# Optimization experiments

Hardware: AMD Instinct MI355X
Metric: run time of the kernel (lower is better)

Reference implementation:

```python
import jax, jax.numpy as jnp
import numpy as np

B, N, D_MODEL = 8, 1024, 512
H, DK = 8, 64
STATIONS = 128
MASK_NEG = -1e9
LN_EPS = 1e-6


def setup_inputs() -> dict:
    key = jax.random.key(0)
    ks = jax.random.split(key, 9)
    return {
        "hidden_states": jax.random.normal(ks[0], (B, N, D_MODEL), dtype=jnp.float32),
        "rpe": jax.random.normal(ks[1], (B, H, N, N), dtype=jnp.float32) * 0.1,
        "Wq": jax.random.normal(ks[2], (H * DK, D_MODEL), dtype=jnp.float32) * 0.02,
        "Wk": jax.random.normal(ks[3], (H * DK, D_MODEL), dtype=jnp.float32) * 0.02,
        "Wv": jax.random.normal(ks[4], (H * DK, D_MODEL), dtype=jnp.float32) * 0.02,
        "fc_w": jax.random.normal(ks[5], (D_MODEL, H * DK), dtype=jnp.float32) * 0.02,
        "fc_b": jnp.zeros((D_MODEL,), dtype=jnp.float32),
        "ln_g": jnp.ones((D_MODEL,), dtype=jnp.float32),
        "ln_b": jnp.zeros((D_MODEL,), dtype=jnp.float32),
    }


def _star_mask(n, stations):
    # q_k_mask: query i attends to key j iff j < stations or i == j
    idx = jnp.arange(n)
    return (idx[None, :] < stations) | (idx[:, None] == idx[None, :])  # [n, n] bool


def reference(hidden_states, rpe, Wq, Wk, Wv, fc_w, fc_b, ln_g, ln_b):
    b, n, _ = hidden_states.shape
    residual = hidden_states
    q = (hidden_states @ Wq.T).reshape(b, n, H, DK)
    k = (hidden_states @ Wk.T).reshape(b, n, H, DK)
    v = (hidden_states @ Wv.T).reshape(b, n, H, DK)
    # sparse star+self-loop QK^T with inline RPE add (dense emulation of QKP_mm_tvm)
    scores = jnp.einsum("bihd,bjhd->bhij", q, k) + rpe  # [b,h,n,n]
    mask = _star_mask(n, STATIONS)
    scores = jnp.where(mask[None, None], scores, MASK_NEG)
    scores = scores / jnp.sqrt(jnp.float32(DK))
    attn = jax.nn.softmax(scores, axis=-1)
    # AttnV_mm_tvm: sparse attn-weights times V
    ctx = jnp.einsum("bhij,bjhd->bihd", attn, v).reshape(b, n, H * DK)
    ctx = ctx @ fc_w.T + fc_b + residual
    mu = jnp.mean(ctx, axis=-1, keepdims=True)
    var = jnp.var(ctx, axis=-1, keepdims=True)
    return (ctx - mu) / jnp.sqrt(var + LN_EPS) * ln_g + ln_b
```

## Files before the change

### kernel.cpp

```cpp
#include <hip/hip_runtime.h>
#include <hip/hip_bf16.h>
#include <math.h>

#define B_  8
#define N_  1024
#define DM  512
#define H_  8
#define DK_ 64
#define ST  128

typedef __attribute__((ext_vector_type(8))) short short8;
typedef __attribute__((ext_vector_type(4))) float floatx4;

#define GLD16(gp, lp)                                                          \
    __builtin_amdgcn_global_load_lds(                                          \
        (const __attribute__((address_space(1))) void*)(gp),                   \
        (__attribute__((address_space(3))) void*)(lp), 16, 0, 0)

__device__ __forceinline__ float b2f(short u) {
    union { unsigned int i; float f; } c;
    c.i = ((unsigned int)(unsigned short)u) << 16;
    return c.f;
}
__device__ __forceinline__ unsigned short f2b(float f) {
    __hip_bfloat16 t = __float2bfloat16(f);
    return *(unsigned short*)&t;
}

struct CastArgs {
    const float* src[5];
    unsigned short* dst[5];
    int n[5];
};

__global__ __launch_bounds__(256)
void cast_bf16_kernel(CastArgs a)
{
    const int j = blockIdx.y;
    const float* __restrict__ s = a.src[j];
    unsigned short* __restrict__ d = a.dst[j];
    const int n = a.n[j];
    int i = (blockIdx.x * 256 + threadIdx.x) * 8;
    if (i >= n) return;
    float4 x0 = *(const float4*)&s[i];
    float4 x1 = *(const float4*)&s[i + 4];
    ushort4 o0, o1;
    o0.x = f2b(x0.x); o0.y = f2b(x0.y); o0.z = f2b(x0.z); o0.w = f2b(x0.w);
    o1.x = f2b(x1.x); o1.y = f2b(x1.y); o1.z = f2b(x1.z); o1.w = f2b(x1.w);
    *(ushort4*)&d[i] = o0;
    *(ushort4*)&d[i + 4] = o1;
}

__device__ __forceinline__
void gemm_core(const unsigned short* __restrict__ A,
               const unsigned short* __restrict__ W,
               int m0, int n0, unsigned short* As, unsigned short* Bs,
               floatx4 acc[4][4])
{
    const int tid = threadIdx.x;
    const int lane = tid & 63;
    const int wave = tid >> 6;
    const int wm = wave >> 1, wn = wave & 1;
    const int srow = tid >> 2;
    const int skq  = (tid & 3) * 8;
    const unsigned short* Ag = A + (size_t)(m0 + srow) * 512 + skq;
    const unsigned short* Bg = W + (size_t)(n0 + srow) * 512 + skq;
    const int mrow = lane & 15;
    const int koff = (lane >> 4) * 8;

    for (int kt = 0; kt < 512; kt += 32) {
        __syncthreads();
        GLD16(Ag + kt,            &As[tid * 8]);
        GLD16(Ag + 64 * 512 + kt, &As[2048 + tid * 8]);
        GLD16(Bg + kt,            &Bs[tid * 8]);
        GLD16(Bg + 64 * 512 + kt, &Bs[2048 + tid * 8]);
        __syncthreads();
        short8 af[4], bf[4];
        #pragma unroll
        for (int t = 0; t < 4; ++t) {
            af[t] = *(const short8*)&As[(wm * 64 + t * 16 + mrow) * 32 + koff];
            bf[t] = *(const short8*)&Bs[(wn * 64 + t * 16 + mrow) * 32 + koff];
        }
        #pragma unroll
        for (int mt = 0; mt < 4; ++mt)
            #pragma unroll
            for (int nt = 0; nt < 4; ++nt)
                acc[mt][nt] = __builtin_amdgcn_mfma_f32_16x16x32_bf16(
                    af[mt], bf[nt], acc[mt][nt], 0, 0, 0);
    }
}

__global__ __launch_bounds__(256)
void qkv_gemm_kernel(const unsigned short* __restrict__ A,
                     const unsigned short* __restrict__ W0,
                     const unsigned short* __restrict__ W1,
                     const unsigned short* __restrict__ W2,
                     unsigned short* __restrict__ qo,
                     unsigned short* __restrict__ ko,
                     unsigned short* __restrict__ vto)
{
    __shared__ __align__(16) unsigned short As[128 * 32];
    __shared__ __align__(16) unsigned short Bs[128 * 32];
    const int by = blockIdx.y;
    const int sel = by >> 2;
    const unsigned short* W = (sel == 0) ? W0 : (sel == 1 ? W1 : W2);
    const int m0 = blockIdx.x * 128;
    const int n0 = (by & 3) * 128;

    floatx4 acc[4][4];
    #pragma unroll
    for (int i = 0; i < 4; ++i)
        #pragma unroll
        for (int j = 0; j < 4; ++j)
            acc[i][j] = (floatx4){0.f, 0.f, 0.f, 0.f};

    gemm_core(A, W, m0, n0, As, Bs, acc);

    const int lane = threadIdx.x & 63;
    const int wave = threadIdx.x >> 6;
    const int wm = wave >> 1, wn = wave & 1;
    const int lx = lane & 15;
    const int rq = (lane >> 4) * 4;

    if (sel == 2) {
        #pragma unroll
        for (int mt = 0; mt < 4; ++mt) {
            const int mrow = m0 + wm * 64 + mt * 16 + rq;
            const int bb = mrow >> 10, tok = mrow & 1023;
            #pragma unroll
            for (int nt = 0; nt < 4; ++nt) {
                const int c = n0 + wn * 64 + nt * 16 + lx;
                const int hh = c >> 6, d = c & 63;
                ushort4 pk;
                pk.x = f2b(acc[mt][nt][0]); pk.y = f2b(acc[mt][nt][1]);
                pk.z = f2b(acc[mt][nt][2]); pk.w = f2b(acc[mt][nt][3]);
                *(ushort4*)&vto[((size_t)(bb * H_ + hh) * DK_ + d) * N_ + tok] = pk;
            }
        }
    } else {
        unsigned short* O = (sel == 0) ? qo : ko;
        #pragma unroll
        for (int mt = 0; mt < 4; ++mt) {
            const int mrow = m0 + wm * 64 + mt * 16 + rq;
            const int bb = mrow >> 10, tok = mrow & 1023;
            #pragma unroll
            for (int nt = 0; nt < 4; ++nt) {
                const int c = n0 + wn * 64 + nt * 16 + lx;
                const int hh = c >> 6, d = c & 63;
                unsigned short* p =
                    O + ((size_t)(bb * H_ + hh) * N_ + tok) * DK_ + d;
                #pragma unroll
                for (int r = 0; r < 4; ++r)
                    p[(size_t)r * DK_] = f2b(acc[mt][nt][r]);
            }
        }
    }
}

__global__ __launch_bounds__(256)
void fc_gemm_kernel(const unsigned short* __restrict__ A,
                    const unsigned short* __restrict__ W,
                    const float* __restrict__ bias,
                    const float* __restrict__ resid,
                    float* __restrict__ C)
{
    __shared__ __align__(16) unsigned short As[128 * 32];
    __shared__ __align__(16) unsigned short Bs[128 * 32];
    const int m0 = blockIdx.x * 128;
    const int n0 = blockIdx.y * 128;

    floatx4 acc[4][4];
    #pragma unroll
    for (int i = 0; i < 4; ++i)
        #pragma unroll
        for (int j = 0; j < 4; ++j)
            acc[i][j] = (floatx4){0.f, 0.f, 0.f, 0.f};

    gemm_core(A, W, m0, n0, As, Bs, acc);

    const int lane = threadIdx.x & 63;
    const int wave = threadIdx.x >> 6;
    const int wm = wave >> 1, wn = wave & 1;
    const int col = n0 + wn * 64 + (lane & 15);
    const int rq  = (lane >> 4) * 4;
    #pragma unroll
    for (int mt = 0; mt < 4; ++mt)
        #pragma unroll
        for (int nt = 0; nt < 4; ++nt) {
            const int c = col + nt * 16;
            const float b = bias[c];
            #pragma unroll
            for (int r = 0; r < 4; ++r) {
                const size_t row = (size_t)(m0 + wm * 64 + mt * 16 + rq + r);
                C[row * 512 + c] = acc[mt][nt][r] + b + resid[row * 512 + c];
            }
        }
}

__global__ __launch_bounds__(256)
void attn_kernel(const unsigned short* __restrict__ qg,
                 const unsigned short* __restrict__ kg,
                 const unsigned short* __restrict__ vtg,
                 const float* __restrict__ rpe,
                 unsigned short* __restrict__ ctx)
{
    __shared__ __align__(16) unsigned short P[64 * 136];

    const int tid  = threadIdx.x;
    const int lane = tid & 63;
    const int w    = tid >> 6;
    const int lx   = lane & 15;
    const int quad = lane >> 4;
    const int qb = blockIdx.x * 64;
    const int h  = blockIdx.y, b = blockIdx.z;
    const int bh = b * H_ + h;
    const unsigned short* qh  = qg  + (size_t)bh * N_ * DK_;
    const unsigned short* kh  = kg  + (size_t)bh * N_ * DK_;
    const unsigned short* vth = vtg + (size_t)bh * DK_ * N_;
    const float* rp = rpe + ((size_t)bh * N_ + qb) * N_;
    const bool has_self = (qb >= ST);

    float sself = -1e30f;
    if (has_self) {
        const int i = qb + w * 16 + lx;
        const unsigned short* qr = qh + (size_t)i * DK_ + quad * 16;
        const unsigned short* kr = kh + (size_t)i * DK_ + quad * 16;
        short8 q0 = *(const short8*)qr, q1 = *(const short8*)(qr + 8);
        short8 k0 = *(const short8*)kr, k1 = *(const short8*)(kr + 8);
        float dot = 0.f;
        #pragma unroll
        for (int j = 0; j < 8; ++j) {
            dot = fmaf(b2f(q0[j]), b2f(k0[j]), dot);
            dot = fmaf(b2f(q1[j]), b2f(k1[j]), dot);
        }
        dot += __shfl_xor(dot, 16, 64);
        dot += __shfl_xor(dot, 32, 64);
        const float rd = rp[(size_t)(w * 16 + lx) * N_ + (qb + w * 16 + lx)];
        sself = (dot + rd) * 0.125f;
    }

    float rv[4][8];
    {
        const float* rbase = rp + (size_t)(w * 16 + quad * 4) * N_ + lx;
        #pragma unroll
        for (int r = 0; r < 4; ++r)
            #pragma unroll
            for (int nt = 0; nt < 8; ++nt)
                rv[r][nt] = rbase[(size_t)r * N_ + nt * 16];
    }

    short8 aq[2];
    {
        const unsigned short* qrow =
            qh + (size_t)(qb + w * 16 + lx) * DK_ + quad * 8;
        aq[0] = *(const short8*)qrow;
        aq[1] = *(const short8*)(qrow + 32);
    }
    floatx4 sacc[8];
    #pragma unroll
    for (int nt = 0; nt < 8; ++nt) sacc[nt] = (floatx4){0.f, 0.f, 0.f, 0.f};
    #pragma unroll
    for (int nt = 0; nt < 8; ++nt) {
        const unsigned short* krow =
            kh + (size_t)(nt * 16 + lx) * DK_ + quad * 8;
        short8 b0 = *(const short8*)krow;
        short8 b1 = *(const short8*)(krow + 32);
        sacc[nt] = __builtin_amdgcn_mfma_f32_16x16x32_bf16(aq[0], b0, sacc[nt], 0, 0, 0);
        sacc[nt] = __builtin_amdgcn_mfma_f32_16x16x32_bf16(aq[1], b1, sacc[nt], 0, 0, 0);
    }

    float l4[4], ps4[4];
    #pragma unroll
    for (int r = 0; r < 4; ++r) {
        float sv[8];
        float mx = -1e30f;
        #pragma unroll
        for (int nt = 0; nt < 8; ++nt) {
            sv[nt] = (sacc[nt][r] + rv[r][nt]) * 0.125f;
            mx = fmaxf(mx, sv[nt]);
        }
        #pragma unroll
        for (int o = 1; o < 16; o <<= 1)
            mx = fmaxf(mx, __shfl_xor(mx, o, 64));
        const float ss = __shfl(sself, quad * 4 + r, 64);
        mx = fmaxf(mx, ss);
        float sum = 0.f;
        #pragma unroll
        for (int nt = 0; nt < 8; ++nt) {
            sv[nt] = __expf(sv[nt] - mx);
            sum += sv[nt];
        }
        #pragma unroll
        for (int o = 1; o < 16; o <<= 1)
            sum += __shfl_xor(sum, o, 64);
        const float ps = has_self ? __expf(ss - mx) : 0.f;
        l4[r] = sum + ps;
        ps4[r] = ps;
        const int row = w * 16 + quad * 4 + r;
        #pragma unroll
        for (int nt = 0; nt < 8; ++nt)
            P[row * 136 + nt * 16 + lx] = f2b(sv[nt]);
    }
    __syncthreads();

    short8 ap[4];
    #pragma unroll
    for (int ks = 0; ks < 4; ++ks)
        ap[ks] = *(const short8*)&P[(w * 16 + lx) * 136 + ks * 32 + quad * 8];
    floatx4 oacc[4];
    #pragma unroll
    for (int nt = 0; nt < 4; ++nt) oacc[nt] = (floatx4){0.f, 0.f, 0.f, 0.f};
    #pragma unroll
    for (int nt = 0; nt < 4; ++nt) {
        const unsigned short* vrow = vth + (size_t)(nt * 16 + lx) * N_;
        #pragma unroll
        for (int ks = 0; ks < 4; ++ks) {
            short8 bv = *(const short8*)(vrow + ks * 32 + quad * 8);
            oacc[nt] = __builtin_amdgcn_mfma_f32_16x16x32_bf16(ap[ks], bv, oacc[nt], 0, 0, 0);
        }
    }

    #pragma unroll
    for (int r = 0; r < 4; ++r) {
        const int i = qb + w * 16 + quad * 4 + r;
        const float inv = 1.0f / l4[r];
        const float ps = ps4[r];
        #pragma unroll
        for (int nt = 0; nt < 4; ++nt) {
            const int d = nt * 16 + lx;
            float o = oacc[nt][r];
            if (has_self)
                o = fmaf(ps, b2f((short)vth[(size_t)d * N_ + i]), o);
            ctx[((size_t)(b * N_) + i) * DM + h * DK_ + d] = f2b(o * inv);
        }
    }
}

__global__ __launch_bounds__(256)
void ln_kernel(float* __restrict__ io, const float* __restrict__ g,
               const float* __restrict__ bb)
{
    const int t = blockIdx.x;
    const int tid = threadIdx.x;
    float* row = io + (size_t)t * DM;
    float2 x = *(const float2*)&row[tid * 2];
    float s  = x.x + x.y;
    float ss = fmaf(x.x, x.x, x.y * x.y);
    #pragma unroll
    for (int o = 1; o < 64; o <<= 1) {
        s  += __shfl_xor(s,  o, 64);
        ss += __shfl_xor(ss, o, 64);
    }
    __shared__ float wsum[4], wsq[4];
    const int w = tid >> 6;
    if ((tid & 63) == 0) { wsum[w] = s; wsq[w] = ss; }
    __syncthreads();
    s  = wsum[0] + wsum[1] + wsum[2] + wsum[3];
    ss = wsq[0]  + wsq[1]  + wsq[2]  + wsq[3];
    const float mean = s * (1.0f / DM);
    const float var  = ss * (1.0f / DM) - mean * mean;
    const float rstd = rsqrtf(var + 1e-6f);
    float2 gg = *(const float2*)&g[tid * 2];
    float2 bv = *(const float2*)&bb[tid * 2];
    x.x = (x.x - mean) * rstd * gg.x + bv.x;
    x.y = (x.y - mean) * rstd * gg.y + bv.y;
    *(float2*)&row[tid * 2] = x;
}

extern "C" void kernel_launch(void* const* d_in, const int* in_sizes, int n_in,
                              void* d_out, int out_size, void* d_ws, size_t ws_size,
                              hipStream_t stream)
{
    (void)in_sizes; (void)n_in; (void)out_size; (void)ws_size;
    const float* hidden = (const float*)d_in[0];
    const float* rpe    = (const float*)d_in[1];
    const float* Wq     = (const float*)d_in[2];
    const float* Wk     = (const float*)d_in[3];
    const float* Wv     = (const float*)d_in[4];
    const float* fc_w   = (const float*)d_in[5];
    const float* fc_b   = (const float*)d_in[6];
    const float* ln_g   = (const float*)d_in[7];
    const float* ln_b   = (const float*)d_in[8];
    float* out = (float*)d_out;
    char* ws = (char*)d_ws;

    const size_t MB = 1024 * 1024;
    unsigned short* hb  = (unsigned short*)(ws + 0 * MB);
    unsigned short* wq  = (unsigned short*)(ws + 8 * MB);
    unsigned short* wk  = (unsigned short*)(ws + 8 * MB + 512 * 1024);
    unsigned short* wv  = (unsigned short*)(ws + 9 * MB);
    unsigned short* wf  = (unsigned short*)(ws + 9 * MB + 512 * 1024);
    unsigned short* qB  = (unsigned short*)(ws + 16 * MB);
    unsigned short* kB  = (unsigned short*)(ws + 24 * MB);
    unsigned short* vtB = (unsigned short*)(ws + 32 * MB);
    unsigned short* cb  = (unsigned short*)(ws + 40 * MB);

    CastArgs ca;
    ca.src[0] = hidden; ca.dst[0] = hb; ca.n[0] = B_ * N_ * DM;
    ca.src[1] = Wq;     ca.dst[1] = wq; ca.n[1] = DM * DM;
    ca.src[2] = Wk;     ca.dst[2] = wk; ca.n[2] = DM * DM;
    ca.src[3] = Wv;     ca.dst[3] = wv; ca.n[3] = DM * DM;
    ca.src[4] = fc_w;   ca.dst[4] = wf; ca.n[4] = DM * DM;
    cast_bf16_kernel<<<dim3(2048, 5), 256, 0, stream>>>(ca);

    qkv_gemm_kernel<<<dim3(64, 12), 256, 0, stream>>>(hb, wq, wk, wv, qB, kB, vtB);
    attn_kernel<<<dim3(16, H_, B_), 256, 0, stream>>>(qB, kB, vtB, rpe, cb);
    fc_gemm_kernel<<<dim3(64, 4), 256, 0, stream>>>(cb, wf, fc_b, hidden, out);
    ln_kernel<<<B_ * N_, 256, 0, stream>>>(out, ln_g, ln_b);
}
```

Baseline: 401.2 us.

## Fuse FC GEMM with LayerNorm and stage self-loop V values in LDS

Replaces the separate fc GEMM and LayerNorm kernels with one kernel. Each 512-thread block computes 32 full output rows across all 512 columns, then reduces mean and variance with shuffles and LDS before writing normalized output. This removes a launch and one full write-then-read of the fp32 output. The attention kernel also stages the diagonal V^T slice into LDS with coalesced loads, replacing scattered per-element global reads in the self-loop term. The trade-off is that the fused GEMM uses 32-row tiles and only 256 blocks, giving less reuse of the weight tiles and possibly lower occupancy.

```diff
diff --git a/kernel.cpp b/kernel.cpp
--- a/kernel.cpp
+++ b/kernel.cpp
@@ -158,46 +158,6 @@
 }
 
 __global__ __launch_bounds__(256)
-void fc_gemm_kernel(const unsigned short* __restrict__ A,
-                    const unsigned short* __restrict__ W,
-                    const float* __restrict__ bias,
-                    const float* __restrict__ resid,
-                    float* __restrict__ C)
-{
-    __shared__ __align__(16) unsigned short As[128 * 32];
-    __shared__ __align__(16) unsigned short Bs[128 * 32];
-    const int m0 = blockIdx.x * 128;
-    const int n0 = blockIdx.y * 128;
-
-    floatx4 acc[4][4];
-    #pragma unroll
-    for (int i = 0; i < 4; ++i)
-        #pragma unroll
-        for (int j = 0; j < 4; ++j)
-            acc[i][j] = (floatx4){0.f, 0.f, 0.f, 0.f};
-
-    gemm_core(A, W, m0, n0, As, Bs, acc);
-
-    const int lane = threadIdx.x & 63;
-    const int wave = threadIdx.x >> 6;
-    const int wm = wave >> 1, wn = wave & 1;
-    const int col = n0 + wn * 64 + (lane & 15);
-    const int rq  = (lane >> 4) * 4;
-    #pragma unroll
-    for (int mt = 0; mt < 4; ++mt)
-        #pragma unroll
-        for (int nt = 0; nt < 4; ++nt) {
-            const int c = col + nt * 16;
-            const float b = bias[c];
-            #pragma unroll
-            for (int r = 0; r < 4; ++r) {
-                const size_t row = (size_t)(m0 + wm * 64 + mt * 16 + rq + r);
-                C[row * 512 + c] = acc[mt][nt][r] + b + resid[row * 512 + c];
-            }
-        }
-}
-
-__global__ __launch_bounds__(256)
 void attn_kernel(const unsigned short* __restrict__ qg,
                  const unsigned short* __restrict__ kg,
                  const unsigned short* __restrict__ vtg,
@@ -205,6 +165,7 @@
                  unsigned short* __restrict__ ctx)
 {
     __shared__ __align__(16) unsigned short P[64 * 136];
+    __shared__ __align__(16) unsigned short Vd[64 * 72];
 
     const int tid  = threadIdx.x;
     const int lane = tid & 63;
@@ -220,6 +181,13 @@
     const float* rp = rpe + ((size_t)bh * N_ + qb) * N_;
     const bool has_self = (qb >= ST);
 
+    if (has_self) {
+        const int d = tid >> 2, t16 = (tid & 3) * 16;
+        const unsigned short* vs = vth + (size_t)d * N_ + qb + t16;
+        *(short8*)&Vd[d * 72 + t16]     = *(const short8*)vs;
+        *(short8*)&Vd[d * 72 + t16 + 8] = *(const short8*)(vs + 8);
+    }
+
     float sself = -1e30f;
     if (has_self) {
         const int i = qb + w * 16 + lx;
@@ -322,7 +290,8 @@
 
     #pragma unroll
     for (int r = 0; r < 4; ++r) {
-        const int i = qb + w * 16 + quad * 4 + r;
+        const int il = w * 16 + quad * 4 + r;
+        const int i = qb + il;
         const float inv = 1.0f / l4[r];
         const float ps = ps4[r];
         #pragma unroll
@@ -330,41 +299,132 @@
             const int d = nt * 16 + lx;
             float o = oacc[nt][r];
             if (has_self)
-                o = fmaf(ps, b2f((short)vth[(size_t)d * N_ + i]), o);
+                o = fmaf(ps, b2f((short)Vd[d * 72 + il]), o);
             ctx[((size_t)(b * N_) + i) * DM + h * DK_ + d] = f2b(o * inv);
         }
     }
 }
 
-__global__ __launch_bounds__(256)
-void ln_kernel(float* __restrict__ io, const float* __restrict__ g,
-               const float* __restrict__ bb)
-{
-    const int t = blockIdx.x;
-    const int tid = threadIdx.x;
-    float* row = io + (size_t)t * DM;
-    float2 x = *(const float2*)&row[tid * 2];
-    float s  = x.x + x.y;
-    float ss = fmaf(x.x, x.x, x.y * x.y);
-    #pragma unroll
-    for (int o = 1; o < 64; o <<= 1) {
-        s  += __shfl_xor(s,  o, 64);
-        ss += __shfl_xor(ss, o, 64);
-    }
-    __shared__ float wsum[4], wsq[4];
-    const int w = tid >> 6;
-    if ((tid & 63) == 0) { wsum[w] = s; wsq[w] = ss; }
+__global__ __launch_bounds__(512)
+void fc_ln_kernel(const unsigned short* __restrict__ A,
+                  const unsigned short* __restrict__ W,
+                  const float* __restrict__ bias,
+                  const float* __restrict__ resid,
+                  const float* __restrict__ g,
+                  const float* __restrict__ bb,
+                  float* __restrict__ out)
+{
+    __shared__ __align__(16) unsigned short As[32 * 32];
+    __shared__ __align__(16) unsigned short Bs[512 * 32];
+    __shared__ float lsum[32][8];
+    __shared__ float lsq[32][8];
+
+    const int tid  = threadIdx.x;
+    const int lane = tid & 63;
+    const int wv   = tid >> 6;
+    const int m0   = blockIdx.x * 32;
+
+    const int srow = tid >> 2;
+    const int skq  = (tid & 3) * 8;
+    const unsigned short* Ag = A + (size_t)(m0 + srow) * 512 + skq;
+    const unsigned short* Bg = W + (size_t)srow * 512 + skq;
+
+    const int mrow = lane & 15;
+    const int koff = (lane >> 4) * 8;
+
+    floatx4 acc[2][4];
+    #pragma unroll
+    for (int i = 0; i < 2; ++i)
+        #pragma unroll
+        for (int j = 0; j < 4; ++j)
+            acc[i][j] = (floatx4){0.f, 0.f, 0.f, 0.f};
+
+    for (int kt = 0; kt < 512; kt += 32) {
+        __syncthreads();
+        if (tid < 128)
+            GLD16(Ag + kt, &As[tid * 8]);
+        #pragma unroll
+        for (int p = 0; p < 4; ++p)
+            GLD16(Bg + (size_t)p * 128 * 512 + kt, &Bs[p * 4096 + tid * 8]);
+        __syncthreads();
+        short8 af[2], bf[4];
+        #pragma unroll
+        for (int t = 0; t < 2; ++t)
+            af[t] = *(const short8*)&As[(t * 16 + mrow) * 32 + koff];
+        #pragma unroll
+        for (int t = 0; t < 4; ++t)
+            bf[t] = *(const short8*)&Bs[(wv * 64 + t * 16 + mrow) * 32 + koff];
+        #pragma unroll
+        for (int mt = 0; mt < 2; ++mt)
+            #pragma unroll
+            for (int nt = 0; nt < 4; ++nt)
+                acc[mt][nt] = __builtin_amdgcn_mfma_f32_16x16x32_bf16(
+                    af[mt], bf[nt], acc[mt][nt], 0, 0, 0);
+    }
+
+    const int quad = lane >> 4;
+    const int lx   = lane & 15;
+    float s[2][4], ss[2][4];
+    #pragma unroll
+    for (int mt = 0; mt < 2; ++mt)
+        #pragma unroll
+        for (int r = 0; r < 4; ++r) { s[mt][r] = 0.f; ss[mt][r] = 0.f; }
+
+    #pragma unroll
+    for (int mt = 0; mt < 2; ++mt)
+        #pragma unroll
+        for (int nt = 0; nt < 4; ++nt) {
+            const int c = wv * 64 + nt * 16 + lx;
+            const float bvv = bias[c];
+            #pragma unroll
+            for (int r = 0; r < 4; ++r) {
+                const size_t row = (size_t)(m0 + mt * 16 + quad * 4 + r);
+                float v = acc[mt][nt][r] + bvv + resid[row * 512 + c];
+                acc[mt][nt][r] = v;
+                s[mt][r] += v;
+                ss[mt][r] = fmaf(v, v, ss[mt][r]);
+            }
+        }
+
+    #pragma unroll
+    for (int o = 1; o < 16; o <<= 1)
+        #pragma unroll
+        for (int mt = 0; mt < 2; ++mt)
+            #pragma unroll
+            for (int r = 0; r < 4; ++r) {
+                s[mt][r]  += __shfl_xor(s[mt][r],  o, 64);
+                ss[mt][r] += __shfl_xor(ss[mt][r], o, 64);
+            }
+    if (lx == 0) {
+        #pragma unroll
+        for (int mt = 0; mt < 2; ++mt)
+            #pragma unroll
+            for (int r = 0; r < 4; ++r) {
+                lsum[mt * 16 + quad * 4 + r][wv] = s[mt][r];
+                lsq [mt * 16 + quad * 4 + r][wv] = ss[mt][r];
+            }
+    }
     __syncthreads();
-    s  = wsum[0] + wsum[1] + wsum[2] + wsum[3];
-    ss = wsq[0]  + wsq[1]  + wsq[2]  + wsq[3];
-    const float mean = s * (1.0f / DM);
-    const float var  = ss * (1.0f / DM) - mean * mean;
-    const float rstd = rsqrtf(var + 1e-6f);
-    float2 gg = *(const float2*)&g[tid * 2];
-    float2 bv = *(const float2*)&bb[tid * 2];
-    x.x = (x.x - mean) * rstd * gg.x + bv.x;
-    x.y = (x.y - mean) * rstd * gg.y + bv.y;
-    *(float2*)&row[tid * 2] = x;
+
+    #pragma unroll
+    for (int mt = 0; mt < 2; ++mt)
+        #pragma unroll
+        for (int r = 0; r < 4; ++r) {
+            const int rl = mt * 16 + quad * 4 + r;
+            float ts = 0.f, tss = 0.f;
+            #pragma unroll
+            for (int u = 0; u < 8; ++u) { ts += lsum[rl][u]; tss += lsq[rl][u]; }
+            const float mean = ts * (1.0f / DM);
+            const float var  = tss * (1.0f / DM) - mean * mean;
+            const float rstd = rsqrtf(var + 1e-6f);
+            const size_t row = (size_t)(m0 + rl);
+            #pragma unroll
+            for (int nt = 0; nt < 4; ++nt) {
+                const int c = wv * 64 + nt * 16 + lx;
+                out[row * 512 + c] =
+                    (acc[mt][nt][r] - mean) * rstd * g[c] + bb[c];
+            }
+        }
 }
 
 extern "C" void kernel_launch(void* const* d_in, const int* in_sizes, int n_in,
@@ -405,6 +465,5 @@
 
     qkv_gemm_kernel<<<dim3(64, 12), 256, 0, stream>>>(hb, wq, wk, wv, qB, kB, vtB);
     attn_kernel<<<dim3(16, H_, B_), 256, 0, stream>>>(qB, kB, vtB, rpe, cb);
-    fc_gemm_kernel<<<dim3(64, 4), 256, 0, stream>>>(cb, wf, fc_b, hidden, out);
-    ln_kernel<<<B_ * N_, 256, 0, stream>>>(out, ln_g, ln_b);
-}
+    fc_ln_kernel<<<dim3(256), 512, 0, stream>>>(cb, wf, fc_b, hidden, ln_g, ln_b, out);
+}
```

Result: faster. 390.1 us (-2.8%).
